# Kernel tuning notes

Hardware: AMD Instinct MI355X
Metric: run time of the kernel (lower is better)

Reference implementation:

```python
import jax, jax.numpy as jnp
import numpy as np

N = 50000
E = 800000
CIN = 32
COUT = 64
DIM = 2
KS = 5                      # kernel size per pseudo-coordinate dim
K = KS ** DIM               # 25 kernel weight matrices
DEGREE = 1
S = (DEGREE + 1) ** DIM     # 4 nonzero B-spline basis products per edge


def _spline_basis(pseudo):
    # pseudo: [E, DIM] in [0, 1]; open linear (degree-1) B-splines per dim.
    v = pseudo * (KS - DEGREE)                              # [E, DIM]
    lo = jnp.floor(v)
    frac = v - lo                                           # [E, DIM]
    lo = jnp.clip(lo.astype(jnp.int32), 0, KS - 2)          # guard p == 1
    bits = (jnp.arange(S)[:, None] >> jnp.arange(DIM)[None, :]) & 1   # [S, DIM]
    # tensor-product basis values: [E, S]
    b = jnp.where(bits[None].astype(bool), frac[:, None, :], 1.0 - frac[:, None, :])
    basis = jnp.prod(b, axis=-1)
    offsets = (KS ** jnp.arange(DIM)).astype(jnp.int32)     # flat-index strides
    wi = jnp.sum((lo[:, None, :] + bits[None]) * offsets[None, None, :], axis=-1)  # [E, S]
    return basis, wi


def setup_inputs() -> dict:
    key = jax.random.key(0)
    k1, k2, k3, k4, k5, k6 = jax.random.split(key, 6)
    bound = 1.0 / np.sqrt(CIN * K)
    x = jax.random.normal(k1, (N, CIN), dtype=jnp.float32)
    edge_index = jax.random.randint(k2, (2, E), 0, N, dtype=jnp.int64)
    pseudo = jax.random.uniform(k3, (E, DIM), dtype=jnp.float32)
    weight = jax.random.uniform(k4, (K, CIN, COUT), minval=-bound, maxval=bound, dtype=jnp.float32)
    root = jax.random.uniform(k5, (CIN, COUT), minval=-bound, maxval=bound, dtype=jnp.float32)
    bias = jax.random.uniform(k6, (COUT,), minval=-bound, maxval=bound, dtype=jnp.float32)
    return {"x": x, "edge_index": edge_index, "pseudo": pseudo,
            "weight": weight, "root": root, "bias": bias}


def reference(x, edge_index, pseudo, weight, root, bias):
    n, cin = x.shape
    cout = weight.shape[-1]
    row = edge_index[0]   # destination nodes (scatter target)
    col = edge_index[1]   # source nodes (gather)
    basis, wi = _spline_basis(pseudo)                       # [E, S], [E, S]
    # Transform every node by every kernel weight matrix: [N, K, Cout]
    y = jnp.einsum('ni,kio->nko', x, weight)
    flat = y.reshape(n * K, cout)
    g = flat[col[:, None] * K + wi]                         # [E, S, Cout] gather
    msg = jnp.einsum('es,eso->eo', basis, g)                # [E, Cout]
    out = jax.ops.segment_sum(msg, row, num_segments=n)     # scatter-add to dst
    deg = jax.ops.segment_sum(jnp.ones((row.shape[0],), dtype=x.dtype), row, num_segments=n)
    out = out / jnp.maximum(deg, 1.0)[:, None]              # degree normalization
    out = out + x @ root + bias                             # root transform + bias
    return out
```

## Files before the change

kernel.cpp:

```cpp
#include <hip/hip_runtime.h>

#define N_NODES 50000
#define E_EDGES 800000
#define CIN     32
#define COUT    64
#define NB      16
#define BCAP    54016
#define NCB     196
#define RCAP    4864
#define KPAD    136
#define SCANB   1024
#define NSCANBLK ((N_NODES + SCANB - 1) / SCANB)
#define EPB     8
#define BBLK    ((E_EDGES + EPB * 256 - 1) / (EPB * 256))
#define XCHUNK  (N_NODES * CIN / 4)

typedef __attribute__((ext_vector_type(8))) short s8v;
typedef __attribute__((ext_vector_type(4))) float f4v;
typedef __attribute__((ext_vector_type(4))) unsigned short u4v;

static __device__ inline unsigned short f2bf(float f) {
    unsigned u = __builtin_bit_cast(unsigned, f);
    u += 0x7fff + ((u >> 16) & 1);
    return (unsigned short)(u >> 16);
}
static __device__ inline float bf2f(unsigned short h) {
    unsigned u = ((unsigned)h) << 16;
    return __builtin_bit_cast(float, u);
}
static __device__ inline unsigned f2bf2(float a, float b) {
    return (unsigned)f2bf(a) | ((unsigned)f2bf(b) << 16);
}


__global__ __launch_bounds__(256) void build_recs(
    const float* __restrict__ x, unsigned short* __restrict__ xbf,
    const int* __restrict__ ei, const float* __restrict__ pseudo,
    int* __restrict__ cursor, int* __restrict__ cursR,
    unsigned long long* __restrict__ recs, unsigned* __restrict__ rp)
{
    {
        const int cb = blockIdx.x * 1024;
#pragma unroll
        for (int k = 0; k < 4; ++k) {
            const int i = cb + k * 256 + threadIdx.x;
            if (i < XCHUNK) {
                f4v v = *(const f4v*)(x + (size_t)i * 4);
                union { unsigned u2[2]; u4v v4; } o;
                o.u2[0] = f2bf2(v[0], v[1]);
                o.u2[1] = f2bf2(v[2], v[3]);
                *(u4v*)(xbf + (size_t)i * 4) = o.v4;
            }
        }
    }

    __shared__ int lh[NB];
    __shared__ int lbase[NB];
    __shared__ int lh2[NCB];
    __shared__ int lbase2[NCB];
    if (threadIdx.x < NB) lh[threadIdx.x] = 0;
    if (threadIdx.x < NCB) lh2[threadIdx.x] = 0;
    __syncthreads();

    const int ebase0 = blockIdx.x * (EPB * 256);
    unsigned long long rcache[EPB];
    int pcache[EPB];
    int pcache2[EPB];

#pragma unroll
    for (int i = 0; i < EPB; ++i) {
        const int e = ebase0 + i * 256 + threadIdx.x;
        pcache[i] = -1; pcache2[i] = -1;
        if (e < E_EDGES) {
            const int row = min(max(ei[e], 0), N_NODES - 1);
            const int col = min(max(ei[E_EDGES + e], 0), N_NODES - 1);
            const float v0 = pseudo[2 * e] * 4.0f, v1 = pseudo[2 * e + 1] * 4.0f;
            const float fl0 = floorf(v0), fl1 = floorf(v1);
            const int lo0 = min(max((int)fl0, 0), 3);
            const int lo1 = min(max((int)fl1, 0), 3);
            const int f0q = min((int)((v0 - fl0) * 65536.0f), 65535);
            const int f1q = min((int)((v1 - fl1) * 65536.0f), 65535);
            const int b = lo0 + 4 * lo1;
            rcache[i] = (unsigned long long)row
                      | ((unsigned long long)col << 16)
                      | ((unsigned long long)f0q << 32)
                      | ((unsigned long long)f1q << 48);
            pcache[i]  = b | (atomicAdd(&lh[b], 1) << 8);
            const int cb = row >> 8;
            pcache2[i] = cb | (atomicAdd(&lh2[cb], 1) << 8);
        }
    }
    __syncthreads();

    if (threadIdx.x < NB)
        lbase[threadIdx.x] = atomicAdd(&cursor[threadIdx.x], lh[threadIdx.x]);
    if (threadIdx.x < NCB)
        lbase2[threadIdx.x] = atomicAdd(&cursR[threadIdx.x], lh2[threadIdx.x]);
    __syncthreads();

#pragma unroll
    for (int i = 0; i < EPB; ++i) {
        if (pcache[i] >= 0) {
            const int b = pcache[i] & 0xFF;
            const int idx = min(lbase[b] + (pcache[i] >> 8), BCAP - 1);
            const unsigned recslot = (unsigned)(b * BCAP + idx);
            recs[recslot] = rcache[i];
            const int cb = pcache2[i] & 0xFF;
            const int idx2 = min(lbase2[cb] + (pcache2[i] >> 8), RCAP - 1);
            const unsigned rowlow = (unsigned)(rcache[i] & 0xFF);
            rp[(size_t)cb * RCAP + idx2] = recslot | (rowlow << 20);
        }
    }
}

__global__ __launch_bounds__(256) void deg_hist(
    const unsigned* __restrict__ rp, const int* __restrict__ cursR,
    int* __restrict__ degi)
{
    __shared__ int h[256];
    h[threadIdx.x] = 0;
    __syncthreads();
    const int cb = blockIdx.x;
    const int cnt = min(cursR[cb], RCAP);
    const unsigned* bp = rp + (size_t)cb * RCAP;
    for (int i = threadIdx.x; i < cnt; i += 256)
        atomicAdd(&h[bp[i] >> 20], 1);
    __syncthreads();
    const int row = cb * 256 + threadIdx.x;
    if (row < N_NODES) degi[row] = h[threadIdx.x];
}

__global__ __launch_bounds__(1024) void scan_blocks(
    const int* __restrict__ degi, int* __restrict__ rowstart, int* __restrict__ bsum)
{
    __shared__ int wsum[16];
    __shared__ int woff[16];
    const int tid = threadIdx.x, lane = tid & 63, wid = tid >> 6;
    const int n = blockIdx.x * SCANB + tid;
    const int v = (n < N_NODES) ? degi[n] : 0;
    int val = v;
#pragma unroll
    for (int off = 1; off < 64; off <<= 1) {
        int t = __shfl_up(val, off);
        if (lane >= off) val += t;
    }
    if (lane == 63) wsum[wid] = val;
    __syncthreads();
    if (tid == 0) {
        int a = 0;
#pragma unroll
        for (int w = 0; w < 16; ++w) { woff[w] = a; a += wsum[w]; }
        bsum[blockIdx.x] = a;
    }
    __syncthreads();
    if (n < N_NODES) rowstart[n] = woff[wid] + (val - v);
}

__global__ __launch_bounds__(1024) void scan_finish(
    int* __restrict__ rowstart, const int* __restrict__ bsum)
{
    const int b = blockIdx.x;
    int off = 0;
    for (int i = 0; i < NSCANBLK; ++i)
        off += (i < b) ? bsum[i] : 0;
    const int n = b * SCANB + threadIdx.x;
    if (n < N_NODES) rowstart[n] += off;
    if (b == NSCANBLK - 1 && threadIdx.x == 0)
        rowstart[N_NODES] = off + bsum[NSCANBLK - 1];
}

__global__ __launch_bounds__(256) void rank_write(
    const unsigned* __restrict__ rp, const int* __restrict__ cursR,
    const int* __restrict__ rowstart, int* __restrict__ dpos)
{
    __shared__ int cur[256];
    const int cb = blockIdx.x;
    const int row = cb * 256 + threadIdx.x;
    cur[threadIdx.x] = (row < N_NODES) ? rowstart[row] : 0;
    __syncthreads();
    const int cnt = min(cursR[cb], RCAP);
    const unsigned* bp = rp + (size_t)cb * RCAP;
    for (int i = threadIdx.x; i < cnt; i += 256) {
        const unsigned e = bp[i];
        const int pos = min(atomicAdd(&cur[e >> 20], 1), E_EDGES - 1);
        dpos[e & 0xFFFFF] = pos;
    }
}

__global__ __launch_bounds__(256, 2) void bucket_mfma_seq(
    const unsigned short* __restrict__ xbf, const float* __restrict__ weight,
    const unsigned long long* __restrict__ recs,
    const int* __restrict__ cursor, const int* __restrict__ degi,
    const int* __restrict__ dpos, unsigned short* __restrict__ msg)
{
    __shared__ short XS[4][16 * KPAD];

    const int lane = threadIdx.x & 63;
    const int wid  = threadIdx.x >> 6;
    const int cell = blockIdx.x & (NB - 1);
    const int wGlob   = (blockIdx.x >> 4) * 4 + wid;
    const int wStride = (gridDim.x >> 4) * 4;
    const int eg = lane >> 2, part = lane & 3;

    const int lo0 = cell & 3, lo1 = cell >> 2;
    const int base = lo0 + 5 * lo1;
    const int offs[4] = {0, 1, 5, 6};
    const int q = lane >> 4;
    const int c = lane & 15;

    s8v bfr[4][4];
#pragma unroll
    for (int s = 0; s < 4; ++s) {
        const float* wp = weight + (size_t)(base + offs[s]) * (CIN * COUT);
#pragma unroll
        for (int nt = 0; nt < 4; ++nt) {
            union { unsigned short u[8]; s8v v; } tmp;
#pragma unroll
            for (int j = 0; j < 8; ++j)
                tmp.u[j] = f2bf(wp[(q * 8 + j) * COUT + nt * 16 + c]);
            bfr[s][nt] = tmp.v;
        }
    }

    const unsigned long long* brec = recs + (size_t)cell * BCAP;
    const int* bdp = dpos + (size_t)cell * BCAP;
    const int cnt    = min(cursor[cell], BCAP);
    const int ntiles = (cnt + 15) >> 4;

    int t = wGlob;
    unsigned long long rec_c = 0;
    int deg_c = 1;
    int dp_c  = 0;
    s8v x_c = {};
    if (t < ntiles) {
        const int ri = min(t * 16 + eg, cnt - 1);
        rec_c = brec[ri];
        deg_c = degi[(int)(rec_c & 0xFFFF)];
        dp_c  = bdp[ri];
        x_c = *(const s8v*)(xbf + (size_t)((rec_c >> 16) & 0xFFFF) * CIN + part * 8);
    }

    for (; t < ntiles; t += wStride) {
        const int tn = t + wStride;
        unsigned long long rec_n = 0;
        int deg_n = 1;
        int dp_n  = 0;
        if (tn < ntiles) {
            const int ri = min(tn * 16 + eg, cnt - 1);
            rec_n = brec[ri];
            deg_n = degi[(int)(rec_n & 0xFFFF)];
            dp_n  = bdp[ri];
        }

        const bool vcur = (t * 16 + eg) < cnt;
        const float f0 = (float)(int)((rec_c >> 32) & 0xFFFF) * (1.0f / 65536.0f);
        const float f1 = (float)(int)((rec_c >> 48) & 0xFFFF) * (1.0f / 65536.0f);
        const float invd = vcur ? (1.0f / (float)max(deg_c, 1)) : 0.0f;
        const float s0 = (1.0f - f0) * (1.0f - f1) * invd;
        const float s1 = f0 * (1.0f - f1) * invd;
        const float s2 = (1.0f - f0) * f1 * invd;
        const float s3 = f0 * f1 * invd;

        {
            union { unsigned short u[8]; s8v v; } xin; xin.v = x_c;
            float xv[8];
#pragma unroll
            for (int j = 0; j < 8; ++j) xv[j] = bf2f(xin.u[j]);
            short* dst = &XS[wid][eg * KPAD + part * 8];
            const float ss[4] = {s0, s1, s2, s3};
#pragma unroll
            for (int s = 0; s < 4; ++s) {
                union { unsigned u2[4]; s8v v; } tmp;
#pragma unroll
                for (int j = 0; j < 8; j += 2)
                    tmp.u2[j >> 1] = f2bf2(ss[s] * xv[j], ss[s] * xv[j + 1]);
                *(s8v*)(dst + s * 32) = tmp.v;
            }
        }
        __builtin_amdgcn_wave_barrier();

        s8v afr[4];
        {
            const short* ap = &XS[wid][c * KPAD + q * 8];
#pragma unroll
            for (int ks = 0; ks < 4; ++ks)
                afr[ks] = *(const s8v*)(ap + ks * 32);
        }
        __builtin_amdgcn_wave_barrier();

        s8v x_n = {};
        if (tn < ntiles)
            x_n = *(const s8v*)(xbf + (size_t)((rec_n >> 16) & 0xFFFF) * CIN + part * 8);

        f4v acc[4];
#pragma unroll
        for (int nt = 0; nt < 4; ++nt) {
            acc[nt] = (f4v){0.f, 0.f, 0.f, 0.f};
#pragma unroll
            for (int ks = 0; ks < 4; ++ks)
                acc[nt] = __builtin_amdgcn_mfma_f32_16x16x32_bf16(
                    afr[ks], bfr[ks][nt], acc[nt], 0, 0, 0);
        }

#pragma unroll
        for (int r = 0; r < 4; ++r) {
            const int m = q * 4 + r;
#pragma unroll
            for (int nt = 0; nt < 4; ++nt)
                XS[wid][m * 64 + nt * 16 + c] = (short)f2bf(acc[nt][r]);
        }
        __builtin_amdgcn_wave_barrier();
        if (vcur) {
            const short* sp = &XS[wid][eg * 64 + part * 8];
            s8v vlo = *(const s8v*)sp;
            s8v vhi = *(const s8v*)(sp + 32);
            unsigned short* dst = msg + (size_t)dp_c * COUT + part * 8;
            *(s8v*)dst = vlo;
            *(s8v*)(dst + 32) = vhi;
        }
        __builtin_amdgcn_wave_barrier();

        rec_c = rec_n; deg_c = deg_n; dp_c = dp_n; x_c = x_n;
    }
}

__global__ __launch_bounds__(256) void gather_seq(
    const unsigned short* __restrict__ msg,
    const int* __restrict__ rowstart, const float* __restrict__ x,
    const float* __restrict__ root, const float* __restrict__ bias,
    float* __restrict__ out)
{
    const int wave   = (blockIdx.x * blockDim.x + threadIdx.x) >> 6;
    const int lane   = threadIdx.x & 63;
    const int nwaves = (gridDim.x * blockDim.x) >> 6;
    const int g = lane >> 3;
    const int c = lane & 7;

    float rfr[4][8];
#pragma unroll
    for (int i = 0; i < 4; ++i) {
        const int ii = g * 4 + i;
        *(f4v*)&rfr[i][0] = *(const f4v*)(root + (size_t)ii * COUT + c * 8);
        *(f4v*)&rfr[i][4] = *(const f4v*)(root + (size_t)ii * COUT + c * 8 + 4);
    }
    float bs[8];
    *(f4v*)&bs[0] = *(const f4v*)(bias + c * 8);
    *(f4v*)&bs[4] = *(const f4v*)(bias + c * 8 + 4);

    for (int n = wave; n < N_NODES; n += nwaves) {
        const int s  = rowstart[n];
        const int e2 = rowstart[n + 1];
        float acc[8] = {0.f, 0.f, 0.f, 0.f, 0.f, 0.f, 0.f, 0.f};

        for (int p = s + g; p < e2; p += 8) {
            union { s8v v; unsigned short u[8]; } mv;
            mv.v = *(const s8v*)(msg + (size_t)p * COUT + c * 8);
#pragma unroll
            for (int j = 0; j < 8; ++j)
                acc[j] += bf2f(mv.u[j]);
        }

        const f4v xv4 = *(const f4v*)(x + (size_t)n * CIN + g * 4);
#pragma unroll
        for (int i = 0; i < 4; ++i) {
            const float xv = xv4[i];
#pragma unroll
            for (int j = 0; j < 8; ++j)
                acc[j] += xv * rfr[i][j];
        }

#pragma unroll
        for (int off = 8; off < 64; off <<= 1) {
#pragma unroll
            for (int j = 0; j < 8; ++j)
                acc[j] += __shfl_xor(acc[j], off);
        }

        if (g == 0) {
            f4v o0, o1;
#pragma unroll
            for (int j = 0; j < 4; ++j) o0[j] = acc[j] + bs[j];
#pragma unroll
            for (int j = 0; j < 4; ++j) o1[j] = acc[4 + j] + bs[4 + j];
            float* op = out + (size_t)n * COUT + c * 8;
            *(f4v*)op = o0;
            *(f4v*)(op + 4) = o1;
        }
    }
}


__global__ __launch_bounds__(256) void count_fb(
    const int* __restrict__ ei, const float* __restrict__ pseudo,
    int* __restrict__ hist, float* __restrict__ deg)
{
    __shared__ int lh[16];
    if (threadIdx.x < 16) lh[threadIdx.x] = 0;
    __syncthreads();
    const int e = blockIdx.x * 256 + threadIdx.x;
    if (e < E_EDGES) {
        int row = min(max(ei[e], 0), N_NODES - 1);
        const float v0 = pseudo[2 * e] * 4.0f, v1 = pseudo[2 * e + 1] * 4.0f;
        const int lo0 = min(max((int)floorf(v0), 0), 3);
        const int lo1 = min(max((int)floorf(v1), 0), 3);
        atomicAdd(&lh[lo0 + 4 * lo1], 1);
        atomicAdd(&deg[row], 1.0f);
    }
    __syncthreads();
    if (threadIdx.x < 16) atomicAdd(&hist[threadIdx.x], lh[threadIdx.x]);
}

__global__ void scan16_fb(const int* __restrict__ hist,
                          int* __restrict__ bstart, int* __restrict__ cursor)
{
    if (threadIdx.x == 0 && blockIdx.x == 0) {
        int acc = 0;
        for (int c = 0; c < 16; ++c) { bstart[c] = acc; cursor[c] = acc; acc += hist[c]; }
    }
}

__global__ __launch_bounds__(256) void scatter_fb(
    const float* __restrict__ pseudo, int* __restrict__ cursor, int* __restrict__ list)
{
    __shared__ int lh[16];
    __shared__ int lbase[16];
    if (threadIdx.x < 16) lh[threadIdx.x] = 0;
    __syncthreads();
    const int e = blockIdx.x * 256 + threadIdx.x;
    int cell = 0, myoff = 0;
    if (e < E_EDGES) {
        const float v0 = pseudo[2 * e] * 4.0f, v1 = pseudo[2 * e + 1] * 4.0f;
        const int lo0 = min(max((int)floorf(v0), 0), 3);
        const int lo1 = min(max((int)floorf(v1), 0), 3);
        cell = lo0 + 4 * lo1;
        myoff = atomicAdd(&lh[cell], 1);
    }
    __syncthreads();
    if (threadIdx.x < 16)
        lbase[threadIdx.x] = atomicAdd(&cursor[threadIdx.x], lh[threadIdx.x]);
    __syncthreads();
    if (e < E_EDGES)
        list[lbase[cell] + myoff] = e;
}

__global__ __launch_bounds__(256, 2) void bucket_mfma_fb(
    const float* __restrict__ x, const int* __restrict__ ei,
    const float* __restrict__ pseudo, const float* __restrict__ weight,
    const int* __restrict__ list, const int* __restrict__ bstart,
    const int* __restrict__ hist, float* __restrict__ out)
{
    __shared__ short XS[4][16 * KPAD];
    const int lane = threadIdx.x & 63;
    const int wid  = threadIdx.x >> 6;
    const int beta = blockIdx.x & 15;
    const int wGlob   = (blockIdx.x >> 4) * 4 + wid;
    const int wStride = (gridDim.x >> 4) * 4;
    const int lo0 = beta & 3, lo1 = beta >> 2;
    const int base = lo0 + 5 * lo1;
    const int offs[4] = {0, 1, 5, 6};
    const int q = lane >> 4, c = lane & 15;

    s8v bfr[4][4];
#pragma unroll
    for (int s = 0; s < 4; ++s) {
        const float* wp = weight + (size_t)(base + offs[s]) * (CIN * COUT);
#pragma unroll
        for (int nt = 0; nt < 4; ++nt) {
            union { unsigned short u[8]; s8v v; } tmp;
#pragma unroll
            for (int j = 0; j < 8; ++j)
                tmp.u[j] = f2bf(wp[(q * 8 + j) * COUT + nt * 16 + c]);
            bfr[s][nt] = tmp.v;
        }
    }
    const int start = bstart[beta], cnt = hist[beta];
    const int ntiles = (cnt + 15) >> 4;

    for (int t = wGlob; t < ntiles; t += wStride) {
        const int ebase = start + t * 16;
        int rowv = 0, colv = 0;
        float b0 = 0.f, b1 = 0.f, b2 = 0.f, b3 = 0.f;
        if (lane < 16 && (t * 16 + lane) < cnt) {
            const int e = list[ebase + lane];
            rowv = min(max(ei[e], 0), N_NODES - 1);
            colv = min(max(ei[E_EDGES + e], 0), N_NODES - 1);
            const float v0 = pseudo[2 * e] * 4.0f, v1 = pseudo[2 * e + 1] * 4.0f;
            const float f0 = v0 - floorf(v0), f1 = v1 - floorf(v1);
            b0 = (1.0f - f0) * (1.0f - f1);
            b1 = f0 * (1.0f - f1);
            b2 = (1.0f - f0) * f1;
            b3 = f0 * f1;
        }
        {
            const int eg = lane >> 2, part = lane & 3;
            const int  gc = __shfl(colv, eg);
            const float ss0 = __shfl(b0, eg), ss1 = __shfl(b1, eg);
            const float ss2 = __shfl(b2, eg), ss3 = __shfl(b3, eg);
            const float ss[4] = {ss0, ss1, ss2, ss3};
            const float* xp = x + (size_t)gc * CIN + part * 8;
            float xv[8];
            *(f4v*)&xv[0] = *(const f4v*)xp;
            *(f4v*)&xv[4] = *(const f4v*)(xp + 4);
            short* dst = &XS[wid][eg * KPAD + part * 8];
#pragma unroll
            for (int s = 0; s < 4; ++s) {
                union { unsigned short u[8]; s8v v; } tmp;
#pragma unroll
                for (int j = 0; j < 8; ++j)
                    tmp.u[j] = f2bf(ss[s] * xv[j]);
                *(s8v*)(dst + s * 32) = tmp.v;
            }
        }
        __builtin_amdgcn_wave_barrier();
        s8v afr[4];
        {
            const short* ap = &XS[wid][c * KPAD + q * 8];
#pragma unroll
            for (int ks = 0; ks < 4; ++ks)
                afr[ks] = *(const s8v*)(ap + ks * 32);
        }
        __builtin_amdgcn_wave_barrier();
        f4v acc[4];
#pragma unroll
        for (int nt = 0; nt < 4; ++nt) {
            acc[nt] = (f4v){0.f, 0.f, 0.f, 0.f};
#pragma unroll
            for (int ks = 0; ks < 4; ++ks)
                acc[nt] = __builtin_amdgcn_mfma_f32_16x16x32_bf16(
                    afr[ks], bfr[ks][nt], acc[nt], 0, 0, 0);
        }
#pragma unroll
        for (int r = 0; r < 4; ++r) {
            const int m = q * 4 + r;
            const int orow = __shfl(rowv, m);
#pragma unroll
            for (int nt = 0; nt < 4; ++nt)
                atomicAdd(&out[(size_t)orow * COUT + nt * 16 + c], acc[nt][r]);
        }
    }
}

__global__ __launch_bounds__(256) void final_fb(
    const float* __restrict__ x, const float* __restrict__ root,
    const float* __restrict__ bias, const float* __restrict__ deg,
    float* __restrict__ out)
{
    const int wave   = (blockIdx.x * blockDim.x + threadIdx.x) >> 6;
    const int lane   = threadIdx.x & 63;
    const int nwaves = (gridDim.x * blockDim.x) >> 6;
    for (int n = wave; n < N_NODES; n += nwaves) {
        const float* xp = x + (size_t)n * CIN;
        float acc = bias[lane];
#pragma unroll
        for (int i = 0; i < CIN; ++i)
            acc += xp[i] * root[i * COUT + lane];
        float dg = deg[n];
        dg = dg > 1.0f ? dg : 1.0f;
        const size_t idx = (size_t)n * COUT + lane;
        out[idx] = out[idx] / dg + acc;
    }
}

extern "C" void kernel_launch(void* const* d_in, const int* in_sizes, int n_in,
                              void* d_out, int out_size, void* d_ws, size_t ws_size,
                              hipStream_t stream) {
    const float* x      = (const float*)d_in[0];
    const int*   ei     = (const int*)d_in[1];
    const float* pseudo = (const float*)d_in[2];
    const float* weight = (const float*)d_in[3];
    const float* root   = (const float*)d_in[4];
    const float* bias   = (const float*)d_in[5];
    float* out = (float*)d_out;

    int* wsI = (int*)d_ws;
    int* cursor16 = wsI;
    int* cursR    = wsI + 32;
    int* degi     = wsI + 256;
    int* rowstart = wsI + 50256;
    int* bsum     = wsI + 100272;
    unsigned long long* recs = (unsigned long long*)((char*)d_ws + 401408);
    unsigned* rp   = (unsigned*)((char*)recs + (size_t)NB * BCAP * 8);
    int* dpos      = (int*)((char*)rp + (size_t)NCB * RCAP * 4);
    unsigned short* xbf = (unsigned short*)((char*)dpos + (size_t)NB * BCAP * 4);
    unsigned short* msg = (unsigned short*)((char*)xbf + (size_t)N_NODES * CIN * 2);
    const size_t needed = 401408 + (size_t)NB * BCAP * 8 + (size_t)NCB * RCAP * 4
                        + (size_t)NB * BCAP * 4 + (size_t)N_NODES * CIN * 2
                        + (size_t)E_EDGES * COUT * 2;

    if (ws_size >= needed) {
        (void)hipMemsetAsync(d_ws, 0, 256 * 4, stream);
        build_recs <<<BBLK, 256, 0, stream>>>(x, xbf, ei, pseudo, cursor16, cursR, recs, rp);
        deg_hist   <<<NCB, 256, 0, stream>>>(rp, cursR, degi);
        scan_blocks<<<NSCANBLK, 1024, 0, stream>>>(degi, rowstart, bsum);
        scan_finish<<<NSCANBLK, 1024, 0, stream>>>(rowstart, bsum);
        rank_write <<<NCB, 256, 0, stream>>>(rp, cursR, rowstart, dpos);
        bucket_mfma_seq<<<16 * 128, 256, 0, stream>>>(
            xbf, weight, recs, cursor16, degi, dpos, msg);
        gather_seq<<<4096, 256, 0, stream>>>(msg, rowstart, x, root, bias, out);
    } else {
        char* w = (char*)d_ws;
        float* degF   = (float*)w;
        int*   histF  = (int*)(w + 200064);
        int*   bstF   = (int*)(w + 200128);
        int*   curF   = (int*)(w + 200192);
        int*   listF  = (int*)(w + 200256);
        const int eblocks = (E_EDGES + 255) / 256;

        (void)hipMemsetAsync(out, 0, sizeof(float) * (size_t)N_NODES * COUT, stream);
        (void)hipMemsetAsync(degF, 0, sizeof(float) * (size_t)N_NODES, stream);
        (void)hipMemsetAsync(histF, 0, 192, stream);

        count_fb      <<<eblocks, 256, 0, stream>>>(ei, pseudo, histF, degF);
        scan16_fb     <<<1, 64, 0, stream>>>(histF, bstF, curF);
        scatter_fb    <<<eblocks, 256, 0, stream>>>(pseudo, curF, listF);
        bucket_mfma_fb<<<16 * 64, 256, 0, stream>>>(x, ei, pseudo, weight, listF,
                                                    bstF, histF, out);
        final_fb      <<<1024, 256, 0, stream>>>(x, root, bias, degF, out);
    }
}
```

Baseline: 179.3 us.

## Swizzle LDS staging, defer degree normalization to gather, use native bf16 convert

Replaces the padded LDS staging layout in the per-edge MFMA kernel with rotated chunk offsets so writes and fragment reads spread across banks. The degree normalization moves from each edge message to the per-node gather, removing a dependent random degi load per edge from the pipelined loop. Float-to-bf16 conversion now uses the compiler's native __bf16 cast. Rounding changes slightly because scaling now happens after bf16 quantization of the message.

```diff
diff --git a/kernel.cpp b/kernel.cpp
--- a/kernel.cpp
+++ b/kernel.cpp
@@ -8,21 +8,20 @@
 #define BCAP    54016
 #define NCB     196
 #define RCAP    4864
-#define KPAD    136
 #define SCANB   1024
 #define NSCANBLK ((N_NODES + SCANB - 1) / SCANB)
 #define EPB     8
 #define BBLK    ((E_EDGES + EPB * 256 - 1) / (EPB * 256))
 #define XCHUNK  (N_NODES * CIN / 4)
+#define KPAD    136
 
 typedef __attribute__((ext_vector_type(8))) short s8v;
 typedef __attribute__((ext_vector_type(4))) float f4v;
 typedef __attribute__((ext_vector_type(4))) unsigned short u4v;
 
 static __device__ inline unsigned short f2bf(float f) {
-    unsigned u = __builtin_bit_cast(unsigned, f);
-    u += 0x7fff + ((u >> 16) & 1);
-    return (unsigned short)(u >> 16);
+    __bf16 b = (__bf16)f;
+    return __builtin_bit_cast(unsigned short, b);
 }
 static __device__ inline float bf2f(unsigned short h) {
     unsigned u = ((unsigned)h) << 16;
@@ -190,10 +189,10 @@
 __global__ __launch_bounds__(256, 2) void bucket_mfma_seq(
     const unsigned short* __restrict__ xbf, const float* __restrict__ weight,
     const unsigned long long* __restrict__ recs,
-    const int* __restrict__ cursor, const int* __restrict__ degi,
+    const int* __restrict__ cursor,
     const int* __restrict__ dpos, unsigned short* __restrict__ msg)
 {
-    __shared__ short XS[4][16 * KPAD];
+    __shared__ short XS[4][2048];
 
     const int lane = threadIdx.x & 63;
     const int wid  = threadIdx.x >> 6;
@@ -222,6 +221,17 @@
         }
     }
 
+    short* const swrow = &XS[wid][eg * 128];
+    int swoff[4];
+#pragma unroll
+    for (int s = 0; s < 4; ++s) swoff[s] = ((4 * s + part + eg) & 15) * 8;
+    const short* const arrow = &XS[wid][c * 128];
+    int aroff[4];
+#pragma unroll
+    for (int ks = 0; ks < 4; ++ks) aroff[ks] = ((4 * ks + q + c) & 15) * 8;
+    const int erlo = eg * 64 + ((part + eg) & 7) * 8;
+    const int erhi = eg * 64 + ((part + 4 + eg) & 7) * 8;
+
     const unsigned long long* brec = recs + (size_t)cell * BCAP;
     const int* bdp = dpos + (size_t)cell * BCAP;
     const int cnt    = min(cursor[cell], BCAP);
@@ -229,13 +239,11 @@
 
     int t = wGlob;
     unsigned long long rec_c = 0;
-    int deg_c = 1;
     int dp_c  = 0;
     s8v x_c = {};
     if (t < ntiles) {
         const int ri = min(t * 16 + eg, cnt - 1);
         rec_c = brec[ri];
-        deg_c = degi[(int)(rec_c & 0xFFFF)];
         dp_c  = bdp[ri];
         x_c = *(const s8v*)(xbf + (size_t)((rec_c >> 16) & 0xFFFF) * CIN + part * 8);
     }
@@ -243,30 +251,26 @@
     for (; t < ntiles; t += wStride) {
         const int tn = t + wStride;
         unsigned long long rec_n = 0;
-        int deg_n = 1;
         int dp_n  = 0;
         if (tn < ntiles) {
             const int ri = min(tn * 16 + eg, cnt - 1);
             rec_n = brec[ri];
-            deg_n = degi[(int)(rec_n & 0xFFFF)];
             dp_n  = bdp[ri];
         }
 
         const bool vcur = (t * 16 + eg) < cnt;
         const float f0 = (float)(int)((rec_c >> 32) & 0xFFFF) * (1.0f / 65536.0f);
         const float f1 = (float)(int)((rec_c >> 48) & 0xFFFF) * (1.0f / 65536.0f);
-        const float invd = vcur ? (1.0f / (float)max(deg_c, 1)) : 0.0f;
-        const float s0 = (1.0f - f0) * (1.0f - f1) * invd;
-        const float s1 = f0 * (1.0f - f1) * invd;
-        const float s2 = (1.0f - f0) * f1 * invd;
-        const float s3 = f0 * f1 * invd;
+        const float s0 = (1.0f - f0) * (1.0f - f1);
+        const float s1 = f0 * (1.0f - f1);
+        const float s2 = (1.0f - f0) * f1;
+        const float s3 = f0 * f1;
 
         {
             union { unsigned short u[8]; s8v v; } xin; xin.v = x_c;
             float xv[8];
 #pragma unroll
             for (int j = 0; j < 8; ++j) xv[j] = bf2f(xin.u[j]);
-            short* dst = &XS[wid][eg * KPAD + part * 8];
             const float ss[4] = {s0, s1, s2, s3};
 #pragma unroll
             for (int s = 0; s < 4; ++s) {
@@ -274,18 +278,15 @@
 #pragma unroll
                 for (int j = 0; j < 8; j += 2)
                     tmp.u2[j >> 1] = f2bf2(ss[s] * xv[j], ss[s] * xv[j + 1]);
-                *(s8v*)(dst + s * 32) = tmp.v;
+                *(s8v*)(swrow + swoff[s]) = tmp.v;
             }
         }
         __builtin_amdgcn_wave_barrier();
 
         s8v afr[4];
-        {
-            const short* ap = &XS[wid][c * KPAD + q * 8];
-#pragma unroll
-            for (int ks = 0; ks < 4; ++ks)
-                afr[ks] = *(const s8v*)(ap + ks * 32);
-        }
+#pragma unroll
+        for (int ks = 0; ks < 4; ++ks)
+            afr[ks] = *(const s8v*)(arrow + aroff[ks]);
         __builtin_amdgcn_wave_barrier();
 
         s8v x_n = {};
@@ -306,21 +307,22 @@
         for (int r = 0; r < 4; ++r) {
             const int m = q * 4 + r;
 #pragma unroll
-            for (int nt = 0; nt < 4; ++nt)
-                XS[wid][m * 64 + nt * 16 + c] = (short)f2bf(acc[nt][r]);
+            for (int nt = 0; nt < 4; ++nt) {
+                const int chunk = (2 * nt + (c >> 3) + m) & 7;
+                XS[wid][m * 64 + chunk * 8 + (c & 7)] = (short)f2bf(acc[nt][r]);
+            }
         }
         __builtin_amdgcn_wave_barrier();
         if (vcur) {
-            const short* sp = &XS[wid][eg * 64 + part * 8];
-            s8v vlo = *(const s8v*)sp;
-            s8v vhi = *(const s8v*)(sp + 32);
+            s8v vlo = *(const s8v*)&XS[wid][erlo];
+            s8v vhi = *(const s8v*)&XS[wid][erhi];
             unsigned short* dst = msg + (size_t)dp_c * COUT + part * 8;
             *(s8v*)dst = vlo;
             *(s8v*)(dst + 32) = vhi;
         }
         __builtin_amdgcn_wave_barrier();
 
-        rec_c = rec_n; deg_c = deg_n; dp_c = dp_n; x_c = x_n;
+        rec_c = rec_n; dp_c = dp_n; x_c = x_n;
     }
 }
 
@@ -359,6 +361,10 @@
             for (int j = 0; j < 8; ++j)
                 acc[j] += bf2f(mv.u[j]);
         }
+
+        const float invd = 1.0f / (float)max(e2 - s, 1);
+#pragma unroll
+        for (int j = 0; j < 8; ++j) acc[j] *= invd;
 
         const f4v xv4 = *(const f4v*)(x + (size_t)n * CIN + g * 4);
 #pragma unroll
@@ -595,7 +601,7 @@
         scan_finish<<<NSCANBLK, 1024, 0, stream>>>(rowstart, bsum);
         rank_write <<<NCB, 256, 0, stream>>>(rp, cursR, rowstart, dpos);
         bucket_mfma_seq<<<16 * 128, 256, 0, stream>>>(
-            xbf, weight, recs, cursor16, degi, dpos, msg);
+            xbf, weight, recs, cursor16, dpos, msg);
         gather_seq<<<4096, 256, 0, stream>>>(msg, rowstart, x, root, bias, out);
     } else {
         char* w = (char*)d_ws;
```

Measured after the change: 173.2 us (median of 2 runs). 1.04x faster.
